# Kernel tuning notes

Measured on AMD Instinct MI355X. Metric: run time of the kernel, lower is better.

The kernel has to match this reference:

```python
import jax, jax.numpy as jnp
import numpy as np

B, H, W, D, DFF = 32, 40, 40, 128, 2048
S = H * W  # 1600
BN_EPS = 1e-5


def setup_inputs() -> dict:
    key = jax.random.key(0)
    ks = jax.random.split(key, 8)
    se = jax.random.normal(ks[2], (H, W, H, W), dtype=jnp.float32)
    se = se + jnp.transpose(se, (2, 3, 0, 1))  # symmetric init as in torch code
    wscale = 0.02
    return {
        "tgt": jax.random.normal(ks[0], (B, H, W, D), dtype=jnp.float32),
        "memory": jax.random.normal(ks[1], (B, H, W, D), dtype=jnp.float32),
        "score_embed": se,
        "w1": jax.random.normal(ks[3], (D, D), dtype=jnp.float32) * wscale,
        "b1": jnp.zeros((D,), jnp.float32),
        "g1": jnp.ones((2 * S,), jnp.float32),
        "be1": jnp.zeros((2 * S,), jnp.float32),
        "w2": jax.random.normal(ks[4], (DFF, 2 * S), dtype=jnp.float32) * wscale,
        "b2": jnp.zeros((DFF,), jnp.float32),
        "g2": jnp.ones((DFF,), jnp.float32),
        "be2": jnp.zeros((DFF,), jnp.float32),
        "w3": jax.random.normal(ks[5], (1, DFF), dtype=jnp.float32) * wscale,
        "b3": jnp.zeros((1,), jnp.float32),
        "g3": jnp.ones((1,), jnp.float32),
        "be3": jnp.zeros((1,), jnp.float32),
    }


def _bn_eval(x, gamma, beta):
    # BatchNorm eval mode with running_mean=0, running_var=1 (as initialized)
    return x * (gamma / jnp.sqrt(1.0 + BN_EPS)) + beta


def _l2norm(x):
    # F.normalize(p=2, dim=-1) with eps=1e-12
    return x / jnp.maximum(jnp.linalg.norm(x, axis=-1, keepdims=True), 1e-12)


def reference(tgt, memory, score_embed, w1, b1, g1, be1, w2, b2, g2, be2, w3, b3, g3, be3):
    b, h, w, d = tgt.shape
    s = h * w
    q = _l2norm(tgt.reshape(b, s, d) @ w1.T + b1)   # [B,S,D]
    k = _l2norm(memory.reshape(b, s, d) @ w1.T + b1)
    gate = jax.nn.sigmoid(score_embed.reshape(s, s))  # [S,S]
    attn = jnp.einsum("bsd,btd->bst", q, k) * gate    # [B,S,S]
    m1 = attn.max(axis=1)  # max over dim 1 -> [B,S]
    m2 = attn.max(axis=2)  # max over dim 2 -> [B,S]
    x = jnp.concatenate([m1, m2], axis=1)  # [B,2S]
    x = _bn_eval(x, g1, be1)
    x = x @ w2.T + b2        # [B,DFF]
    x = jax.nn.relu(_bn_eval(x, g2, be2))
    x = x @ w3.T + b3        # [B,1]
    x = _bn_eval(x, g3, be3)
    return x.squeeze(-1)     # [B]
```

## Files before the change

### kernel.cpp

```cpp
#include <hip/hip_runtime.h>
#include <hip/hip_bf16.h>

#define BB 32
#define SS 1600
#define DD 128
#define DFFN 2048
#define S2N 3200
#define RS 136

typedef __attribute__((ext_vector_type(8))) short short8;
typedef __attribute__((ext_vector_type(4))) float floatx4;
typedef unsigned int u32;
typedef unsigned short u16;

__device__ __forceinline__ u32 encf(float f) {
  u32 u = __float_as_uint(f);
  return (u & 0x80000000u) ? ~u : (u | 0x80000000u);
}
__device__ __forceinline__ float decf(u32 e) {
  u32 u = (e & 0x80000000u) ? (e & 0x7fffffffu) : ~e;
  return __uint_as_float(u);
}
__device__ __forceinline__ u16 f2b(float x) {
  __hip_bfloat16 h = __float2bfloat16(x);
  return __builtin_bit_cast(u16, h);
}

__global__ __launch_bounds__(256) void k_init(const float* __restrict__ se,
                                              float* __restrict__ gT,
                                              u32* __restrict__ m1u,
                                              u32* __restrict__ m2u) {
  __shared__ float t64[64][65];
  int bx = blockIdx.x % 25, by = blockIdx.x / 25;
  int r0 = by * 64, c0 = bx * 64;
  int tr = threadIdx.x >> 4, tc4 = (threadIdx.x & 15) * 4;
  for (int p = 0; p < 4; ++p) {
    int r = p * 16 + tr;
    float4 v = *(const float4*)(se + (size_t)(r0 + r) * SS + c0 + tc4);
    t64[r][tc4 + 0] = 1.f / (1.f + __expf(-v.x));
    t64[r][tc4 + 1] = 1.f / (1.f + __expf(-v.y));
    t64[r][tc4 + 2] = 1.f / (1.f + __expf(-v.z));
    t64[r][tc4 + 3] = 1.f / (1.f + __expf(-v.w));
  }
  __syncthreads();
  for (int p = 0; p < 4; ++p) {
    int c = p * 16 + tr;
    float4 o;
    o.x = t64[tc4 + 0][c];
    o.y = t64[tc4 + 1][c];
    o.z = t64[tc4 + 2][c];
    o.w = t64[tc4 + 3][c];
    *(float4*)(gT + (size_t)(c0 + c) * SS + r0 + tc4) = o;
  }
  int i = blockIdx.x * 256 + threadIdx.x;
  if (i < BB * SS) {
    m1u[i] = 0u;
    m2u[i] = 0u;
  }
}

__global__ __launch_bounds__(256) void k_proj(const float* __restrict__ tgt,
                                              const float* __restrict__ memin,
                                              const float* __restrict__ w1,
                                              const float* __restrict__ b1,
                                              u16* __restrict__ qb, u16* __restrict__ kb) {
  __shared__ u16 sA[128 * RS];
  __shared__ u16 sB[128 * RS];
  __shared__ float sq[128];
  int tid = threadIdx.x;
  long row0 = (long)blockIdx.x * 128;
  const float* src;
  u16* dst;
  if (row0 < (long)BB * SS) { src = tgt + row0 * DD; dst = qb + row0 * DD; }
  else { src = memin + (row0 - (long)BB * SS) * DD; dst = kb + (row0 - (long)BB * SS) * DD; }

  for (int p = 0; p < 16; ++p) {
    int r = p * 8 + (tid >> 5);
    int c4 = (tid & 31) * 4;
    float4 v = *(const float4*)(src + r * DD + c4);
    u32 p0 = (u32)f2b(v.x) | ((u32)f2b(v.y) << 16);
    u32 p1 = (u32)f2b(v.z) | ((u32)f2b(v.w) << 16);
    *(u32*)&sA[r * RS + c4] = p0;
    *(u32*)&sA[r * RS + c4 + 2] = p1;
    float4 w = *(const float4*)(w1 + r * DD + c4);
    u32 q0 = (u32)f2b(w.x) | ((u32)f2b(w.y) << 16);
    u32 q1 = (u32)f2b(w.z) | ((u32)f2b(w.w) << 16);
    *(u32*)&sB[r * RS + c4] = q0;
    *(u32*)&sB[r * RS + c4 + 2] = q1;
  }
  if (tid < 128) sq[tid] = 0.f;
  __syncthreads();

  int lane = tid & 63, wv = tid >> 6;
  int wr = wv >> 1, wc = wv & 1;
  int l15 = lane & 15, lg = lane >> 4;

  floatx4 acc[4][4];
  for (int mi = 0; mi < 4; ++mi)
    for (int ni = 0; ni < 4; ++ni) acc[mi][ni] = (floatx4){0.f, 0.f, 0.f, 0.f};

  for (int kc = 0; kc < 4; ++kc) {
    int k0 = kc * 32 + lg * 8;
    short8 af[4], bfr[4];
    for (int mi = 0; mi < 4; ++mi) af[mi] = *(const short8*)&sA[(wr * 64 + mi * 16 + l15) * RS + k0];
    for (int ni = 0; ni < 4; ++ni) bfr[ni] = *(const short8*)&sB[(wc * 64 + ni * 16 + l15) * RS + k0];
    for (int mi = 0; mi < 4; ++mi)
      for (int ni = 0; ni < 4; ++ni)
        acc[mi][ni] = __builtin_amdgcn_mfma_f32_16x16x32_bf16(af[mi], bfr[ni], acc[mi][ni], 0, 0, 0);
  }

  float bvals[4];
  for (int ni = 0; ni < 4; ++ni) bvals[ni] = b1[wc * 64 + ni * 16 + l15];
  for (int mi = 0; mi < 4; ++mi)
    for (int r = 0; r < 4; ++r) {
      float s = 0.f;
      for (int ni = 0; ni < 4; ++ni) {
        float v = acc[mi][ni][r] + bvals[ni];
        acc[mi][ni][r] = v;
        s += v * v;
      }
      s += __shfl_xor(s, 1); s += __shfl_xor(s, 2);
      s += __shfl_xor(s, 4); s += __shfl_xor(s, 8);
      if (l15 == 0) atomicAdd(&sq[wr * 64 + mi * 16 + lg * 4 + r], s);
    }
  __syncthreads();

  for (int mi = 0; mi < 4; ++mi)
    for (int r = 0; r < 4; ++r) {
      int row = wr * 64 + mi * 16 + lg * 4 + r;
      float scale = 1.f / fmaxf(sqrtf(sq[row]), 1e-12f);
      for (int ni = 0; ni < 4; ++ni)
        sA[row * RS + wc * 64 + ni * 16 + l15] = f2b(acc[mi][ni][r] * scale);
    }
  __syncthreads();
  for (int p = 0; p < 16; ++p) {
    int r = p * 8 + (tid >> 5);
    int c4 = (tid & 31) * 4;
    uint2 val = *(const uint2*)&sA[r * RS + c4];
    *(uint2*)(dst + r * DD + c4) = val;
  }
}

__global__ __launch_bounds__(256) void k_attn(const u16* __restrict__ qb,
                                              const u16* __restrict__ kb,
                                              const float* __restrict__ gT,
                                              u32* __restrict__ m1u, u32* __restrict__ m2u) {
  __shared__ u16 sQ[128 * RS];
  __shared__ u16 sK[128 * RS];
  __shared__ float scmax[2][128];
  __shared__ float srmax[2][128];
  int tid = threadIdx.x;
  int b = blockIdx.z;
  int t0 = (blockIdx.x == 12) ? (SS - 128) : blockIdx.x * 128;
  int s0 = (blockIdx.y == 12) ? (SS - 128) : blockIdx.y * 128;
  int lane = tid & 63, wv = tid >> 6;
  int wr = wv >> 1, wc = wv & 1;
  int l15 = lane & 15, lg = lane >> 4;
  const size_t base = (size_t)b * SS * DD;

  {
    int r = tid >> 4;
    int c8 = (tid & 15) * 8;
    for (int p = 0; p < 8; ++p) {
      int rr = p * 16 + r;
      *(uint4*)&sQ[rr * RS + c8] = *(const uint4*)(qb + base + (size_t)(s0 + rr) * DD + c8);
      *(uint4*)&sK[rr * RS + c8] = *(const uint4*)(kb + base + (size_t)(t0 + rr) * DD + c8);
    }
  }

  floatx4 g4[4][4];
  {
    int srow0 = s0 + wr * 64 + lg * 4;
    int tc0 = t0 + wc * 64 + l15;
    for (int mi = 0; mi < 4; ++mi)
      for (int ni = 0; ni < 4; ++ni)
        g4[mi][ni] = *(const floatx4*)(gT + (size_t)(tc0 + ni * 16) * SS + srow0 + mi * 16);
  }
  __syncthreads();

  floatx4 acc[4][4];
  for (int mi = 0; mi < 4; ++mi)
    for (int ni = 0; ni < 4; ++ni) acc[mi][ni] = (floatx4){0.f, 0.f, 0.f, 0.f};
  for (int kc = 0; kc < 4; ++kc) {
    int k0 = kc * 32 + lg * 8;
    short8 af[4], bfr[4];
    for (int mi = 0; mi < 4; ++mi) af[mi] = *(const short8*)&sQ[(wr * 64 + mi * 16 + l15) * RS + k0];
    for (int ni = 0; ni < 4; ++ni) bfr[ni] = *(const short8*)&sK[(wc * 64 + ni * 16 + l15) * RS + k0];
    for (int mi = 0; mi < 4; ++mi)
      for (int ni = 0; ni < 4; ++ni)
        acc[mi][ni] = __builtin_amdgcn_mfma_f32_16x16x32_bf16(af[mi], bfr[ni], acc[mi][ni], 0, 0, 0);
  }

  float rmax[4][4];
  for (int mi = 0; mi < 4; ++mi)
    for (int r = 0; r < 4; ++r) rmax[mi][r] = -1e30f;
  float cmax[4];
  for (int ni = 0; ni < 4; ++ni) cmax[ni] = -1e30f;

  for (int mi = 0; mi < 4; ++mi)
    for (int ni = 0; ni < 4; ++ni)
      for (int r = 0; r < 4; ++r) {
        float v = acc[mi][ni][r] * g4[mi][ni][r];
        rmax[mi][r] = fmaxf(rmax[mi][r], v);
        cmax[ni] = fmaxf(cmax[ni], v);
      }

  for (int ni = 0; ni < 4; ++ni) {
    cmax[ni] = fmaxf(cmax[ni], __shfl_xor(cmax[ni], 16));
    cmax[ni] = fmaxf(cmax[ni], __shfl_xor(cmax[ni], 32));
  }
  if (lane < 16)
    for (int ni = 0; ni < 4; ++ni) scmax[wr][wc * 64 + ni * 16 + l15] = cmax[ni];

  for (int mi = 0; mi < 4; ++mi)
    for (int r = 0; r < 4; ++r) {
      float v = rmax[mi][r];
      v = fmaxf(v, __shfl_xor(v, 1));
      v = fmaxf(v, __shfl_xor(v, 2));
      v = fmaxf(v, __shfl_xor(v, 4));
      v = fmaxf(v, __shfl_xor(v, 8));
      if (l15 == 0) srmax[wc][wr * 64 + mi * 16 + lg * 4 + r] = v;
    }
  __syncthreads();

  if (tid < 128) {
    float v = fmaxf(scmax[0][tid], scmax[1][tid]);
    atomicMax(&m1u[b * SS + t0 + tid], encf(v));
  } else {
    int i = tid - 128;
    float v = fmaxf(srmax[0][i], srmax[1][i]);
    atomicMax(&m2u[b * SS + s0 + i], encf(v));
  }
}

__global__ __launch_bounds__(256) void k_bn1(const u32* __restrict__ m1u,
                                             const u32* __restrict__ m2u,
                                             const float* __restrict__ g1,
                                             const float* __restrict__ be1,
                                             float* __restrict__ xb) {
  int i = blockIdx.x * 256 + threadIdx.x;
  if (i >= BB * S2N) return;
  int bb = i / S2N, c = i % S2N;
  u32 e = (c < SS) ? m1u[bb * SS + c] : m2u[bb * SS + (c - SS)];
  float v = decf(e);
  float gs = g1[c] * rsqrtf(1.f + 1e-5f);
  xb[i] = v * gs + be1[c];
}

__global__ __launch_bounds__(256) void k_gemm2(const float* __restrict__ xb,
                                               const float* __restrict__ w2,
                                               float* __restrict__ hacc) {
  int tid = threadIdx.x;
  int lane = tid & 63, wv = tid >> 6;
  int f0 = blockIdx.x * 32 + wv * 8;
  int cs = blockIdx.y;
  int cr0 = cs * 800;
  int c_sub = lane & 15, bq = lane >> 4;
  float acc[8][8];
  for (int a = 0; a < 8; ++a)
    for (int c = 0; c < 8; ++c) acc[a][c] = 0.f;
  const float4 z4 = {0.f, 0.f, 0.f, 0.f};
  for (int it = 0; it < 13; ++it) {
    int coff = it * 64 + c_sub * 4;
    bool ok = coff < 800;
    int c = cr0 + coff;
    float4 w4[8], x4[8];
    for (int jf = 0; jf < 8; ++jf)
      w4[jf] = ok ? *(const float4*)(w2 + (size_t)(f0 + jf) * S2N + c) : z4;
    for (int j = 0; j < 8; ++j)
      x4[j] = ok ? *(const float4*)(xb + (size_t)(bq * 8 + j) * S2N + c) : z4;
    for (int jf = 0; jf < 8; ++jf)
      for (int j = 0; j < 8; ++j) {
        float a = acc[jf][j];
        a = fmaf(w4[jf].x, x4[j].x, a);
        a = fmaf(w4[jf].y, x4[j].y, a);
        a = fmaf(w4[jf].z, x4[j].z, a);
        a = fmaf(w4[jf].w, x4[j].w, a);
        acc[jf][j] = a;
      }
  }
  for (int jf = 0; jf < 8; ++jf)
    for (int j = 0; j < 8; ++j) {
      float v = acc[jf][j];
      v += __shfl_xor(v, 1); v += __shfl_xor(v, 2);
      v += __shfl_xor(v, 4); v += __shfl_xor(v, 8);
      acc[jf][j] = v;
    }
  if ((lane & 15) == 0) {
    for (int jf = 0; jf < 8; ++jf)
      for (int j = 0; j < 8; ++j) {
        int b = bq * 8 + j;
        hacc[((size_t)cs * BB + b) * DFFN + f0 + jf] = acc[jf][j];
      }
  }
}

__global__ __launch_bounds__(256) void k_final(const float* __restrict__ hacc,
                                               const float* __restrict__ b2,
                                               const float* __restrict__ g2,
                                               const float* __restrict__ be2,
                                               const float* __restrict__ w3,
                                               const float* __restrict__ b3,
                                               const float* __restrict__ g3,
                                               const float* __restrict__ be3,
                                               float* __restrict__ out) {
  __shared__ float wsum[4];
  int b = blockIdx.x;
  int tid = threadIdx.x;
  float bnc = rsqrtf(1.f + 1e-5f);
  float part = 0.f;
  for (int f = tid; f < DFFN; f += 256) {
    float s = hacc[((size_t)0 * BB + b) * DFFN + f] + hacc[((size_t)1 * BB + b) * DFFN + f] +
              hacc[((size_t)2 * BB + b) * DFFN + f] + hacc[((size_t)3 * BB + b) * DFFN + f];
    s += b2[f];
    s = s * (g2[f] * bnc) + be2[f];
    s = fmaxf(s, 0.f);
    part += s * w3[f];
  }
  for (int m = 1; m < 64; m <<= 1) part += __shfl_xor(part, m);
  if ((tid & 63) == 0) wsum[tid >> 6] = part;
  __syncthreads();
  if (tid == 0) {
    float tot = wsum[0] + wsum[1] + wsum[2] + wsum[3] + b3[0];
    out[b] = tot * (g3[0] * bnc) + be3[0];
  }
}

extern "C" void kernel_launch(void* const* d_in, const int* in_sizes, int n_in,
                              void* d_out, int out_size, void* d_ws, size_t ws_size,
                              hipStream_t stream) {
  const float* tgt = (const float*)d_in[0];
  const float* memin = (const float*)d_in[1];
  const float* se = (const float*)d_in[2];
  const float* w1 = (const float*)d_in[3];
  const float* b1 = (const float*)d_in[4];
  const float* g1 = (const float*)d_in[5];
  const float* be1 = (const float*)d_in[6];
  const float* w2 = (const float*)d_in[7];
  const float* b2 = (const float*)d_in[8];
  const float* g2 = (const float*)d_in[9];
  const float* be2 = (const float*)d_in[10];
  const float* w3 = (const float*)d_in[11];
  const float* b3 = (const float*)d_in[12];
  const float* g3 = (const float*)d_in[13];
  const float* be3 = (const float*)d_in[14];
  float* out = (float*)d_out;

  char* ws = (char*)d_ws;
  const size_t OFF_GT = 0;
  const size_t OFF_QB = 10240000;
  const size_t OFF_KB = OFF_QB + 13107200;
  const size_t OFF_M1 = OFF_KB + 13107200;
  const size_t OFF_M2 = OFF_M1 + 204800;
  const size_t OFF_XB = OFF_M2 + 204800;
  const size_t OFF_HA = OFF_XB + 409600;
  const size_t NEEDED = OFF_HA + (size_t)4 * BB * DFFN * 4;
  if (ws_size < NEEDED) return;

  float* gT = (float*)(ws + OFF_GT);
  u16* qb = (u16*)(ws + OFF_QB);
  u16* kb = (u16*)(ws + OFF_KB);
  u32* m1u = (u32*)(ws + OFF_M1);
  u32* m2u = (u32*)(ws + OFF_M2);
  float* xb = (float*)(ws + OFF_XB);
  float* hacc = (float*)(ws + OFF_HA);

  k_init<<<625, 256, 0, stream>>>(se, gT, m1u, m2u);
  k_proj<<<800, 256, 0, stream>>>(tgt, memin, w1, b1, qb, kb);
  k_attn<<<dim3(13, 13, 32), 256, 0, stream>>>(qb, kb, gT, m1u, m2u);
  k_bn1<<<400, 256, 0, stream>>>(m1u, m2u, g1, be1, xb);
  k_gemm2<<<dim3(64, 4), 256, 0, stream>>>(xb, w2, hacc);
  k_final<<<32, 256, 0, stream>>>(hacc, b2, g2, be2, w3, b3, g3, be3, out);
}
```

Baseline: 167.5 us.

## Store gate in bf16, load Q fragments to registers, remap attn grid, fuse BN1 into GEMM2

The sigmoid gate table is now written and read as bf16, which halves the gate traffic that k_attn reads for every batch. k_attn loads Q fragments straight into registers instead of staging them in LDS, and adds a launch_bounds occupancy hint. It also flattens the grid with an XCD-aware interleave so tiles from the same batch land near each other. The separate BN1 kernel is removed: GEMM2 decodes the atomic max values and applies the BN scale and shift inline, dropping a launch and the xb buffer. The bf16 gate adds rounding error to the attention scores before the max.

```diff
diff --git a/kernel.cpp b/kernel.cpp
--- a/kernel.cpp
+++ b/kernel.cpp
@@ -25,9 +25,10 @@
   __hip_bfloat16 h = __float2bfloat16(x);
   return __builtin_bit_cast(u16, h);
 }
+__device__ __forceinline__ float b2f(u16 h) { return __uint_as_float(((u32)h) << 16); }
 
 __global__ __launch_bounds__(256) void k_init(const float* __restrict__ se,
-                                              float* __restrict__ gT,
+                                              u16* __restrict__ gTb,
                                               u32* __restrict__ m1u,
                                               u32* __restrict__ m2u) {
   __shared__ float t64[64][65];
@@ -45,12 +46,12 @@
   __syncthreads();
   for (int p = 0; p < 4; ++p) {
     int c = p * 16 + tr;
-    float4 o;
-    o.x = t64[tc4 + 0][c];
-    o.y = t64[tc4 + 1][c];
-    o.z = t64[tc4 + 2][c];
-    o.w = t64[tc4 + 3][c];
-    *(float4*)(gT + (size_t)(c0 + c) * SS + r0 + tc4) = o;
+    ushort4 o;
+    o.x = f2b(t64[tc4 + 0][c]);
+    o.y = f2b(t64[tc4 + 1][c]);
+    o.z = f2b(t64[tc4 + 2][c]);
+    o.w = f2b(t64[tc4 + 3][c]);
+    *(ushort4*)(gTb + (size_t)(c0 + c) * SS + r0 + tc4) = o;
   }
   int i = blockIdx.x * 256 + threadIdx.x;
   if (i < BB * SS) {
@@ -141,40 +142,40 @@
   }
 }
 
-__global__ __launch_bounds__(256) void k_attn(const u16* __restrict__ qb,
-                                              const u16* __restrict__ kb,
-                                              const float* __restrict__ gT,
-                                              u32* __restrict__ m1u, u32* __restrict__ m2u) {
-  __shared__ u16 sQ[128 * RS];
+__global__ __launch_bounds__(256, 3) void k_attn(const u16* __restrict__ qb,
+                                                 const u16* __restrict__ kb,
+                                                 const u16* __restrict__ gTb,
+                                                 u32* __restrict__ m1u, u32* __restrict__ m2u) {
   __shared__ u16 sK[128 * RS];
   __shared__ float scmax[2][128];
   __shared__ float srmax[2][128];
   int tid = threadIdx.x;
-  int b = blockIdx.z;
-  int t0 = (blockIdx.x == 12) ? (SS - 128) : blockIdx.x * 128;
-  int s0 = (blockIdx.y == 12) ? (SS - 128) : blockIdx.y * 128;
+  int n = blockIdx.x;
+  int id = (n & 7) * 676 + (n >> 3);
+  int b = id / 169;
+  int r2 = id - b * 169;
+  int sy = r2 / 13, tx = r2 - sy * 13;
+  int s0 = min(sy * 128, SS - 128);
+  int t0 = min(tx * 128, SS - 128);
   int lane = tid & 63, wv = tid >> 6;
   int wr = wv >> 1, wc = wv & 1;
   int l15 = lane & 15, lg = lane >> 4;
   const size_t base = (size_t)b * SS * DD;
 
+  short8 qf[4][4];
   {
-    int r = tid >> 4;
+    const u16* qp = qb + base + (size_t)(s0 + wr * 64 + l15) * DD + lg * 8;
+    for (int mi = 0; mi < 4; ++mi)
+      for (int kc = 0; kc < 4; ++kc)
+        qf[mi][kc] = *(const short8*)(qp + mi * 16 * DD + kc * 32);
+  }
+  {
+    int rr0 = tid >> 4;
     int c8 = (tid & 15) * 8;
-    for (int p = 0; p < 8; ++p) {
-      int rr = p * 16 + r;
-      *(uint4*)&sQ[rr * RS + c8] = *(const uint4*)(qb + base + (size_t)(s0 + rr) * DD + c8);
-      *(uint4*)&sK[rr * RS + c8] = *(const uint4*)(kb + base + (size_t)(t0 + rr) * DD + c8);
-    }
-  }
-
-  floatx4 g4[4][4];
-  {
-    int srow0 = s0 + wr * 64 + lg * 4;
-    int tc0 = t0 + wc * 64 + l15;
-    for (int mi = 0; mi < 4; ++mi)
-      for (int ni = 0; ni < 4; ++ni)
-        g4[mi][ni] = *(const floatx4*)(gT + (size_t)(tc0 + ni * 16) * SS + srow0 + mi * 16);
+    const u16* kp = kb + base + (size_t)(t0 + rr0) * DD + c8;
+    u16* sp = &sK[rr0 * RS + c8];
+    for (int p = 0; p < 8; ++p)
+      *(uint4*)(sp + p * 16 * RS) = *(const uint4*)(kp + (size_t)p * 16 * DD);
   }
   __syncthreads();
 
@@ -183,12 +184,11 @@
     for (int ni = 0; ni < 4; ++ni) acc[mi][ni] = (floatx4){0.f, 0.f, 0.f, 0.f};
   for (int kc = 0; kc < 4; ++kc) {
     int k0 = kc * 32 + lg * 8;
-    short8 af[4], bfr[4];
-    for (int mi = 0; mi < 4; ++mi) af[mi] = *(const short8*)&sQ[(wr * 64 + mi * 16 + l15) * RS + k0];
+    short8 bfr[4];
     for (int ni = 0; ni < 4; ++ni) bfr[ni] = *(const short8*)&sK[(wc * 64 + ni * 16 + l15) * RS + k0];
     for (int mi = 0; mi < 4; ++mi)
       for (int ni = 0; ni < 4; ++ni)
-        acc[mi][ni] = __builtin_amdgcn_mfma_f32_16x16x32_bf16(af[mi], bfr[ni], acc[mi][ni], 0, 0, 0);
+        acc[mi][ni] = __builtin_amdgcn_mfma_f32_16x16x32_bf16(qf[mi][kc], bfr[ni], acc[mi][ni], 0, 0, 0);
   }
 
   float rmax[4][4];
@@ -197,13 +197,21 @@
   float cmax[4];
   for (int ni = 0; ni < 4; ++ni) cmax[ni] = -1e30f;
 
-  for (int mi = 0; mi < 4; ++mi)
-    for (int ni = 0; ni < 4; ++ni)
-      for (int r = 0; r < 4; ++r) {
-        float v = acc[mi][ni][r] * g4[mi][ni][r];
-        rmax[mi][r] = fmaxf(rmax[mi][r], v);
-        cmax[ni] = fmaxf(cmax[ni], v);
-      }
+  int srow0 = s0 + wr * 64 + lg * 4;
+  int tc0 = t0 + wc * 64 + l15;
+  for (int mi = 0; mi < 4; ++mi)
+    for (int ni = 0; ni < 4; ++ni) {
+      ushort4 ge = *(const ushort4*)(gTb + (size_t)(tc0 + ni * 16) * SS + srow0 + mi * 16);
+      float v0 = acc[mi][ni][0] * b2f(ge.x);
+      float v1 = acc[mi][ni][1] * b2f(ge.y);
+      float v2 = acc[mi][ni][2] * b2f(ge.z);
+      float v3 = acc[mi][ni][3] * b2f(ge.w);
+      rmax[mi][0] = fmaxf(rmax[mi][0], v0);
+      rmax[mi][1] = fmaxf(rmax[mi][1], v1);
+      rmax[mi][2] = fmaxf(rmax[mi][2], v2);
+      rmax[mi][3] = fmaxf(rmax[mi][3], v3);
+      cmax[ni] = fmaxf(cmax[ni], fmaxf(fmaxf(v0, v1), fmaxf(v2, v3)));
+    }
 
   for (int ni = 0; ni < 4; ++ni) {
     cmax[ni] = fmaxf(cmax[ni], __shfl_xor(cmax[ni], 16));
@@ -233,21 +241,10 @@
   }
 }
 
-__global__ __launch_bounds__(256) void k_bn1(const u32* __restrict__ m1u,
-                                             const u32* __restrict__ m2u,
-                                             const float* __restrict__ g1,
-                                             const float* __restrict__ be1,
-                                             float* __restrict__ xb) {
-  int i = blockIdx.x * 256 + threadIdx.x;
-  if (i >= BB * S2N) return;
-  int bb = i / S2N, c = i % S2N;
-  u32 e = (c < SS) ? m1u[bb * SS + c] : m2u[bb * SS + (c - SS)];
-  float v = decf(e);
-  float gs = g1[c] * rsqrtf(1.f + 1e-5f);
-  xb[i] = v * gs + be1[c];
-}
-
-__global__ __launch_bounds__(256) void k_gemm2(const float* __restrict__ xb,
+__global__ __launch_bounds__(256) void k_gemm2(const u32* __restrict__ m1u,
+                                               const u32* __restrict__ m2u,
+                                               const float* __restrict__ g1,
+                                               const float* __restrict__ be1,
                                                const float* __restrict__ w2,
                                                float* __restrict__ hacc) {
   int tid = threadIdx.x;
@@ -255,7 +252,10 @@
   int f0 = blockIdx.x * 32 + wv * 8;
   int cs = blockIdx.y;
   int cr0 = cs * 800;
+  const u32* msrc = (cs < 2) ? m1u : m2u;
+  int mcol0 = cr0 - ((cs < 2) ? 0 : SS);
   int c_sub = lane & 15, bq = lane >> 4;
+  const float bnc = rsqrtf(1.f + 1e-5f);
   float acc[8][8];
   for (int a = 0; a < 8; ++a)
     for (int c = 0; c < 8; ++c) acc[a][c] = 0.f;
@@ -263,12 +263,24 @@
   for (int it = 0; it < 13; ++it) {
     int coff = it * 64 + c_sub * 4;
     bool ok = coff < 800;
-    int c = cr0 + coff;
+    int cg = cr0 + coff;
     float4 w4[8], x4[8];
+    float4 gv = ok ? *(const float4*)(g1 + cg) : z4;
+    float4 bv = ok ? *(const float4*)(be1 + cg) : z4;
+    gv.x *= bnc; gv.y *= bnc; gv.z *= bnc; gv.w *= bnc;
     for (int jf = 0; jf < 8; ++jf)
-      w4[jf] = ok ? *(const float4*)(w2 + (size_t)(f0 + jf) * S2N + c) : z4;
-    for (int j = 0; j < 8; ++j)
-      x4[j] = ok ? *(const float4*)(xb + (size_t)(bq * 8 + j) * S2N + c) : z4;
+      w4[jf] = ok ? *(const float4*)(w2 + (size_t)(f0 + jf) * S2N + cg) : z4;
+    for (int j = 0; j < 8; ++j) {
+      if (ok) {
+        uint4 e = *(const uint4*)(msrc + (size_t)(bq * 8 + j) * SS + mcol0 + coff);
+        x4[j].x = decf(e.x) * gv.x + bv.x;
+        x4[j].y = decf(e.y) * gv.y + bv.y;
+        x4[j].z = decf(e.z) * gv.z + bv.z;
+        x4[j].w = decf(e.w) * gv.w + bv.w;
+      } else {
+        x4[j] = z4;
+      }
+    }
     for (int jf = 0; jf < 8; ++jf)
       for (int j = 0; j < 8; ++j) {
         float a = acc[jf][j];
@@ -348,27 +360,24 @@
 
   char* ws = (char*)d_ws;
   const size_t OFF_GT = 0;
-  const size_t OFF_QB = 10240000;
+  const size_t OFF_QB = 5120000;
   const size_t OFF_KB = OFF_QB + 13107200;
   const size_t OFF_M1 = OFF_KB + 13107200;
   const size_t OFF_M2 = OFF_M1 + 204800;
-  const size_t OFF_XB = OFF_M2 + 204800;
-  const size_t OFF_HA = OFF_XB + 409600;
+  const size_t OFF_HA = OFF_M2 + 204800;
   const size_t NEEDED = OFF_HA + (size_t)4 * BB * DFFN * 4;
   if (ws_size < NEEDED) return;
 
-  float* gT = (float*)(ws + OFF_GT);
+  u16* gTb = (u16*)(ws + OFF_GT);
   u16* qb = (u16*)(ws + OFF_QB);
   u16* kb = (u16*)(ws + OFF_KB);
   u32* m1u = (u32*)(ws + OFF_M1);
   u32* m2u = (u32*)(ws + OFF_M2);
-  float* xb = (float*)(ws + OFF_XB);
   float* hacc = (float*)(ws + OFF_HA);
 
-  k_init<<<625, 256, 0, stream>>>(se, gT, m1u, m2u);
+  k_init<<<625, 256, 0, stream>>>(se, gTb, m1u, m2u);
   k_proj<<<800, 256, 0, stream>>>(tgt, memin, w1, b1, qb, kb);
-  k_attn<<<dim3(13, 13, 32), 256, 0, stream>>>(qb, kb, gT, m1u, m2u);
-  k_bn1<<<400, 256, 0, stream>>>(m1u, m2u, g1, be1, xb);
-  k_gemm2<<<dim3(64, 4), 256, 0, stream>>>(xb, w2, hacc);
+  k_attn<<<5408, 256, 0, stream>>>(qb, kb, gTb, m1u, m2u);
+  k_gemm2<<<dim3(64, 4), 256, 0, stream>>>(m1u, m2u, g1, be1, w2, hacc);
   k_final<<<32, 256, 0, stream>>>(hacc, b2, g2, be2, w3, b3, g3, be3, out);
 }
```

New measurement: 187.2 us. 11.7% more time.
